# Kernel tuning notes

Hardware: AMD Instinct MI355X
Metric: run time of the kernel (lower is better)

The kernel has to match this reference:

```python
import jax, jax.numpy as jnp
import numpy as np
import math

DM, DP, P = 1024, 128, 256
B, S = 8, 4096

def setup_inputs() -> dict:
    key = jax.random.key(0)
    ks = jax.random.split(key, 7)
    sd = lambda fan_in: 1.0 / math.sqrt(fan_in)
    return {
        "x": jax.random.normal(ks[0], (B, S, DM), jnp.float32),
        "prim_embeds": jax.random.normal(ks[1], (P, DP), jnp.float32),
        "Wq": jax.random.normal(ks[2], (DP, DM), jnp.float32) * sd(DM),
        "Wk": jax.random.normal(ks[3], (DP, DP), jnp.float32) * sd(DP),
        "Wv": jax.random.normal(ks[4], (DP, DP), jnp.float32) * sd(DP),
        "Wo": jax.random.normal(ks[5], (DM, DP), jnp.float32) * sd(DP),
        "gate_w": jax.random.normal(ks[6], (1, DM), jnp.float32) * sd(DM),
        "gate_b": jnp.zeros((1,), jnp.float32),
    }

def reference(x, prim_embeds, Wq, Wk, Wv, Wo, gate_w, gate_b):
    # q: [B,S,dp]; k,v: [P,dp]
    q = jnp.einsum('bsm,pm->bsp', x, Wq)          # p here = d_prim
    k = prim_embeds @ Wk.T                         # [P, dp]
    v = prim_embeds @ Wv.T                         # [P, dp]
    scale = 1.0 / math.sqrt(q.shape[-1])
    scores = jnp.einsum('bsd,pd->bsp', q, k) * scale  # [B,S,P]
    attn = jax.nn.softmax(scores, axis=-1)
    ctx = jnp.einsum('bsp,pd->bsd', attn, v)       # [B,S,dp]
    out = jnp.einsum('bsd,md->bsm', ctx, Wo)       # [B,S,dm]
    gate = jax.nn.sigmoid(jnp.einsum('bsm,om->bso', x, gate_w) + gate_b)  # [B,S,1]
    return gate * out
```

## Files before the change

kernel.cpp:

```cpp
#include <hip/hip_runtime.h>
#include <hip/hip_bf16.h>

typedef unsigned short ushort_t;
typedef __attribute__((ext_vector_type(8))) short short8;
typedef __attribute__((ext_vector_type(8))) unsigned short ushort8;
typedef __attribute__((ext_vector_type(4))) float f32x4;

#define MFMA16(a,b,c) __builtin_amdgcn_mfma_f32_16x16x32_bf16((a),(b),(c),0,0,0)

__device__ __forceinline__ ushort_t f2bf(float f) {
  unsigned int u = __builtin_bit_cast(unsigned int, f);
  u += 0x7FFFu + ((u >> 16) & 1u);
  return (ushort_t)(u >> 16);
}
__device__ __forceinline__ unsigned int pack2bf(float a, float b) {
  unsigned int ua = __builtin_bit_cast(unsigned int, a);
  unsigned int ub = __builtin_bit_cast(unsigned int, b);
  ua += 0x7FFFu + ((ua >> 16) & 1u);
  ub += 0x7FFFu + ((ub >> 16) & 1u);
  return (ua >> 16) | (ub & 0xFFFF0000u);
}

#define DMd 1024
#define DPd 128
#define PPd 256

#define KWQ_OFF 0
#define KWQ_SIZE (8*17*4*512)
#define VWO_OFF KWQ_SIZE
#define VWO_SIZE (64*8*512)
#define KV_BYTE_OFF ((size_t)(KWQ_SIZE + VWO_SIZE) * 2)

__global__ __launch_bounds__(256) void prep1_kernel(
    const float* __restrict__ prim, const float* __restrict__ Wk,
    const float* __restrict__ Wv, ushort_t* __restrict__ ws) {
  __shared__ __align__(16) float Wl[128 * 132];
  __shared__ __align__(16) float pl[2 * 128];
  const int t = threadIdx.x;
  const int mat = blockIdx.x & 1;
  const int p0 = (blockIdx.x >> 1) * 2;
  const float* W = mat ? Wv : Wk;
  #pragma unroll
  for (int i = 0; i < 16; ++i) {
    int w = (i * 256 + t) * 4;
    int row = w >> 7, col = w & 127;
    *(float4*)&Wl[row * 132 + col] = *(const float4*)(W + w);
  }
  if (t < 64) {
    int row = t >> 5, col = (t & 31) * 4;
    *(float4*)&pl[row * 128 + col] = *(const float4*)(prim + (p0 + row) * 128 + col);
  }
  __syncthreads();
  const int d = t & 127, slot = t >> 7;
  float a0 = 0.f, a1 = 0.f, a2 = 0.f, a3 = 0.f;
  #pragma unroll
  for (int j = 0; j < 128; j += 4) {
    float4 w4 = *(const float4*)&Wl[d * 132 + j];
    float4 p4 = *(const float4*)&pl[slot * 128 + j];
    a0 += w4.x * p4.x; a1 += w4.y * p4.y; a2 += w4.z * p4.z; a3 += w4.w * p4.w;
  }
  float r = (a0 + a1) + (a2 + a3);
  float* kf = (float*)((char*)ws + KV_BYTE_OFF);
  float* vT = kf + 32768;
  if (mat == 0) kf[(p0 + slot) * 128 + d] = r;
  else          vT[d * 256 + p0 + slot] = r;
}

__global__ __launch_bounds__(256) void prep2_kernel(
    const float* __restrict__ Wq, const float* __restrict__ Wo,
    const float* __restrict__ gate_w, ushort_t* __restrict__ ws) {
  const float* kf = (const float*)((const char*)ws + KV_BYTE_OFF);
  const float* vT = kf + 32768;
  __shared__ __align__(16) float tile[8 * 128];
  const int b = blockIdx.x, t = threadIdx.x;
  float acc[8];
  #pragma unroll
  for (int j = 0; j < 8; ++j) acc[j] = 0.f;
  if (b < 136) {
    const int pt = b >> 2, ms = b & 3;
    const int p0 = pt * 8;
    const int p  = p0 + (t >> 5);
    const int m0 = ms * 256 + (t & 31) * 8;
    if (p0 < 256) {
      *(float4*)&tile[t * 4] = *(const float4*)(kf + p0 * 128 + t * 4);
      __syncthreads();
      const float* kp = &tile[(t >> 5) * 128];
      for (int d = 0; d < 128; d += 4) {
        float4 kv = *(const float4*)&kp[d];
        float4 qa0 = *(const float4*)(Wq + (d + 0) * 1024 + m0);
        float4 qb0 = *(const float4*)(Wq + (d + 0) * 1024 + m0 + 4);
        float4 qa1 = *(const float4*)(Wq + (d + 1) * 1024 + m0);
        float4 qb1 = *(const float4*)(Wq + (d + 1) * 1024 + m0 + 4);
        float4 qa2 = *(const float4*)(Wq + (d + 2) * 1024 + m0);
        float4 qb2 = *(const float4*)(Wq + (d + 2) * 1024 + m0 + 4);
        float4 qa3 = *(const float4*)(Wq + (d + 3) * 1024 + m0);
        float4 qb3 = *(const float4*)(Wq + (d + 3) * 1024 + m0 + 4);
        acc[0] += kv.x*qa0.x + kv.y*qa1.x + kv.z*qa2.x + kv.w*qa3.x;
        acc[1] += kv.x*qa0.y + kv.y*qa1.y + kv.z*qa2.y + kv.w*qa3.y;
        acc[2] += kv.x*qa0.z + kv.y*qa1.z + kv.z*qa2.z + kv.w*qa3.z;
        acc[3] += kv.x*qa0.w + kv.y*qa1.w + kv.z*qa2.w + kv.w*qa3.w;
        acc[4] += kv.x*qb0.x + kv.y*qb1.x + kv.z*qb2.x + kv.w*qb3.x;
        acc[5] += kv.x*qb0.y + kv.y*qb1.y + kv.z*qb2.y + kv.w*qb3.y;
        acc[6] += kv.x*qb0.z + kv.y*qb1.z + kv.z*qb2.z + kv.w*qb3.z;
        acc[7] += kv.x*qb0.w + kv.y*qb1.w + kv.z*qb2.w + kv.w*qb3.w;
      }
    } else if (p == 256) {
      #pragma unroll
      for (int j = 0; j < 8; ++j) acc[j] = gate_w[m0 + j];
    }
    const int c = m0 >> 7, ct = p >> 4, k4 = (m0 >> 5) & 3;
    const int row = ((m0 >> 3) & 3) * 16 + (p & 15);
    ushort8 u;
    #pragma unroll
    for (int j = 0; j < 8; ++j) u[j] = f2bf(acc[j]);
    *(ushort8*)&ws[KWQ_OFF + ((size_t)(c * 17 + ct) * 4 + k4) * 512 + (size_t)row * 8] = u;
  } else {
    const int mb  = b - 136;
    const int m0t = mb * 8;
    const int m   = m0t + (t >> 5);
    const int p8  = (t & 31) * 8;
    *(float4*)&tile[t * 4] = *(const float4*)(Wo + (size_t)m0t * 128 + t * 4);
    __syncthreads();
    const float* wo = &tile[(t >> 5) * 128];
    for (int d = 0; d < 128; d += 4) {
      float4 wv = *(const float4*)&wo[d];
      float4 va0 = *(const float4*)(vT + (d + 0) * 256 + p8);
      float4 vb0 = *(const float4*)(vT + (d + 0) * 256 + p8 + 4);
      float4 va1 = *(const float4*)(vT + (d + 1) * 256 + p8);
      float4 vb1 = *(const float4*)(vT + (d + 1) * 256 + p8 + 4);
      float4 va2 = *(const float4*)(vT + (d + 2) * 256 + p8);
      float4 vb2 = *(const float4*)(vT + (d + 2) * 256 + p8 + 4);
      float4 va3 = *(const float4*)(vT + (d + 3) * 256 + p8);
      float4 vb3 = *(const float4*)(vT + (d + 3) * 256 + p8 + 4);
      acc[0] += wv.x*va0.x + wv.y*va1.x + wv.z*va2.x + wv.w*va3.x;
      acc[1] += wv.x*va0.y + wv.y*va1.y + wv.z*va2.y + wv.w*va3.y;
      acc[2] += wv.x*va0.z + wv.y*va1.z + wv.z*va2.z + wv.w*va3.z;
      acc[3] += wv.x*va0.w + wv.y*va1.w + wv.z*va2.w + wv.w*va3.w;
      acc[4] += wv.x*vb0.x + wv.y*vb1.x + wv.z*vb2.x + wv.w*vb3.x;
      acc[5] += wv.x*vb0.y + wv.y*vb1.y + wv.z*vb2.y + wv.w*vb3.y;
      acc[6] += wv.x*vb0.z + wv.y*vb1.z + wv.z*vb2.z + wv.w*vb3.z;
      acc[7] += wv.x*vb0.w + wv.y*vb1.w + wv.z*vb2.w + wv.w*vb3.w;
    }
    const int ctg = m >> 4, k8 = p8 >> 5;
    const int row = ((p8 >> 3) & 3) * 16 + (m & 15);
    ushort8 u;
    #pragma unroll
    for (int j = 0; j < 8; ++j) u[j] = f2bf(acc[j]);
    *(ushort8*)&ws[VWO_OFF + ((size_t)(ctg * 8 + k8) * 512) + (size_t)row * 8] = u;
  }
}

#define LDX 136
#define LDSLAB 264

__global__ __launch_bounds__(256, 4) void scores_kernel(
    const float* __restrict__ x, const float* __restrict__ gate_b,
    const ushort_t* __restrict__ ws, float* __restrict__ out)
{
  __shared__ __align__(16) char smem[2 * 32 * LDX * 2 + 32 * 4 * 4 * 2 + 32 * 4];
  ushort_t* xt0      = (ushort_t*)smem;
  ushort_t* xt1      = xt0 + 32 * LDX;
  ushort_t* slab     = (ushort_t*)smem;
  float*    pmax     = (float*)(smem + 2 * 32 * LDX * 2);
  float*    psum     = pmax + 128;
  float*    gate_lds = psum + 128;

  const int t = threadIdx.x, wid = t >> 6, lane = t & 63;
  const int quad = lane >> 4, l16 = lane & 15;
  const int tok0 = blockIdx.x * 32;

  f32x4 acc[2][5];
  #pragma unroll
  for (int rt = 0; rt < 2; ++rt)
    #pragma unroll
    for (int ctl = 0; ctl < 5; ++ctl) acc[rt][ctl] = (f32x4){0.f,0.f,0.f,0.f};

  #pragma unroll
  for (int i = 0; i < 4; ++i) {
    int flat = i * 1024 + t * 4;
    int row = flat >> 7, col = flat & 127;
    float4 fv = *(const float4*)(x + (size_t)(tok0 + row) * 1024 + col);
    unsigned int pk0 = pack2bf(fv.x, fv.y), pk1 = pack2bf(fv.z, fv.w);
    *(unsigned long long*)&xt0[row * LDX + col] =
        (unsigned long long)pk0 | ((unsigned long long)pk1 << 32);
  }
  __syncthreads();

  for (int c = 0; c < 8; ++c) {
    ushort_t* cur = (c & 1) ? xt1 : xt0;
    ushort_t* nxt = (c & 1) ? xt0 : xt1;
    float4 fv[4];
    if (c < 7) {
      #pragma unroll
      for (int i = 0; i < 4; ++i) {
        int flat = i * 1024 + t * 4;
        int row = flat >> 7, col = flat & 127;
        fv[i] = *(const float4*)(x + (size_t)(tok0 + row) * 1024 + (c + 1) * 128 + col);
      }
    }
    #pragma unroll
    for (int k4 = 0; k4 < 4; ++k4) {
      short8 a[2];
      #pragma unroll
      for (int rt = 0; rt < 2; ++rt)
        a[rt] = *(const short8*)&cur[(rt * 16 + l16) * LDX + k4 * 32 + quad * 8];
      #pragma unroll
      for (int ctl = 0; ctl < 5; ++ctl) {
        if (ctl == 4 && wid != 3) continue;
        const int ct = wid * 4 + ctl;
        short8 bfr = *(const short8*)&ws[KWQ_OFF +
            ((size_t)(c * 17 + ct) * 4 + k4) * 512 + (size_t)lane * 8];
        #pragma unroll
        for (int rt = 0; rt < 2; ++rt) acc[rt][ctl] = MFMA16(a[rt], bfr, acc[rt][ctl]);
      }
    }
    if (c < 7) {
      #pragma unroll
      for (int i = 0; i < 4; ++i) {
        int flat = i * 1024 + t * 4;
        int row = flat >> 7, col = flat & 127;
        unsigned int pk0 = pack2bf(fv[i].x, fv[i].y), pk1 = pack2bf(fv[i].z, fv[i].w);
        *(unsigned long long*)&nxt[row * LDX + col] =
            (unsigned long long)pk0 | ((unsigned long long)pk1 << 32);
      }
      __syncthreads();
    }
  }

  const float SC = 0.08838834764831845f * 1.44269504088896f;
  #pragma unroll
  for (int rt = 0; rt < 2; ++rt)
    #pragma unroll
    for (int r = 0; r < 4; ++r) {
      float m = acc[rt][0][r];
      #pragma unroll
      for (int ctl = 1; ctl < 4; ++ctl) m = fmaxf(m, acc[rt][ctl][r]);
      #pragma unroll
      for (int msk = 1; msk < 16; msk <<= 1) m = fmaxf(m, __shfl_xor(m, msk, 64));
      if (l16 == 0) pmax[(rt * 16 + quad * 4 + r) * 4 + wid] = m;
    }
  __syncthreads();
  float Mf[2][4];
  #pragma unroll
  for (int rt = 0; rt < 2; ++rt)
    #pragma unroll
    for (int r = 0; r < 4; ++r) {
      f32x4 pm = *(f32x4*)&pmax[(rt * 16 + quad * 4 + r) * 4];
      Mf[rt][r] = fmaxf(fmaxf(pm[0], pm[1]), fmaxf(pm[2], pm[3]));
    }
  float Sm[2][4];
  #pragma unroll
  for (int rt = 0; rt < 2; ++rt)
    #pragma unroll
    for (int r = 0; r < 4; ++r) Sm[rt][r] = 0.f;
  #pragma unroll
  for (int rt = 0; rt < 2; ++rt)
    #pragma unroll
    for (int ctl = 0; ctl < 4; ++ctl)
      #pragma unroll
      for (int r = 0; r < 4; ++r) {
        float e = exp2f((acc[rt][ctl][r] - Mf[rt][r]) * SC);
        acc[rt][ctl][r] = e;
        Sm[rt][r] += e;
      }
  #pragma unroll
  for (int rt = 0; rt < 2; ++rt)
    #pragma unroll
    for (int r = 0; r < 4; ++r) {
      #pragma unroll
      for (int msk = 1; msk < 16; msk <<= 1) Sm[rt][r] += __shfl_xor(Sm[rt][r], msk, 64);
    }
  if (l16 == 0) {
    #pragma unroll
    for (int rt = 0; rt < 2; ++rt)
      #pragma unroll
      for (int r = 0; r < 4; ++r)
        psum[(rt * 16 + quad * 4 + r) * 4 + wid] = Sm[rt][r];
    if (wid == 3) {
      float gb = gate_b[0];
      #pragma unroll
      for (int rt = 0; rt < 2; ++rt)
        #pragma unroll
        for (int r = 0; r < 4; ++r) {
          float lg = acc[rt][4][r] + gb;
          gate_lds[rt * 16 + quad * 4 + r] = 1.f / (1.f + __expf(-lg));
        }
    }
  }
  __syncthreads();
  float scl[2][4];
  #pragma unroll
  for (int rt = 0; rt < 2; ++rt)
    #pragma unroll
    for (int r = 0; r < 4; ++r) {
      f32x4 ps = *(f32x4*)&psum[(rt * 16 + quad * 4 + r) * 4];
      float g = gate_lds[rt * 16 + quad * 4 + r];
      scl[rt][r] = g / (ps[0] + ps[1] + ps[2] + ps[3]);
    }

  #pragma unroll
  for (int rt = 0; rt < 2; ++rt)
    #pragma unroll
    for (int ctl = 0; ctl < 4; ++ctl)
      #pragma unroll
      for (int r = 0; r < 4; ++r)
        slab[(rt * 16 + quad * 4 + r) * LDSLAB + (wid * 4 + ctl) * 16 + l16] =
            f2bf(acc[rt][ctl][r] * scl[rt][r]);
  __syncthreads();

  #pragma unroll
  for (int j = 0; j < 4; ++j) {
    int flat = j * 1024 + t * 4;
    int row = flat >> 7, col = flat & 127;
    uint4 v = *(const uint4*)&slab[row * LDSLAB + col * 2];
    *(uint4*)&out[(size_t)(tok0 + row) * 1024 + 896 + col] = v;
  }
}

__global__ __launch_bounds__(256, 4) void out_kernel(
    const ushort_t* __restrict__ ws, float* __restrict__ out)
{
  __shared__ __align__(16) ushort_t slab[32 * LDSLAB];
  const int t = threadIdx.x, wid = t >> 6, lane = t & 63;
  const int quad = lane >> 4, l16 = lane & 15;
  const int tok0 = blockIdx.x * 32;

  #pragma unroll
  for (int j = 0; j < 4; ++j) {
    int flat = j * 1024 + t * 4;
    int row = flat >> 7, col = flat & 127;
    uint4 v = *(const uint4*)&out[(size_t)(tok0 + row) * 1024 + 896 + col];
    *(uint4*)&slab[row * LDSLAB + col * 2] = v;
  }
  __syncthreads();

  short8 af[2][8];
  #pragma unroll
  for (int rt = 0; rt < 2; ++rt)
    #pragma unroll
    for (int k8 = 0; k8 < 8; ++k8)
      af[rt][k8] = *(const short8*)&slab[(rt * 16 + l16) * LDSLAB + k8 * 32 + quad * 8];

  const int n0 = wid * 256;
  for (int nt = 0; nt < 16; ++nt) {
    const int ctg = (n0 >> 4) + nt;
    short8 bf[8];
    #pragma unroll
    for (int k8 = 0; k8 < 8; ++k8)
      bf[k8] = *(const short8*)&ws[VWO_OFF + ((size_t)(ctg * 8 + k8) * 512) + (size_t)lane * 8];
    f32x4 oa[2];
    #pragma unroll
    for (int rt = 0; rt < 2; ++rt) oa[rt] = (f32x4){0.f,0.f,0.f,0.f};
    #pragma unroll
    for (int rt = 0; rt < 2; ++rt)
      #pragma unroll
      for (int k8 = 0; k8 < 8; ++k8)
        oa[rt] = MFMA16(af[rt][k8], bf[k8], oa[rt]);
    #pragma unroll
    for (int rt = 0; rt < 2; ++rt)
      #pragma unroll
      for (int r = 0; r < 4; ++r)
        __builtin_nontemporal_store(oa[rt][r],
            &out[(size_t)(tok0 + rt * 16 + quad * 4 + r) * 1024 + n0 + nt * 16 + l16]);
  }
}

extern "C" void kernel_launch(void* const* d_in, const int* in_sizes, int n_in,
                              void* d_out, int out_size, void* d_ws, size_t ws_size,
                              hipStream_t stream) {
  const float* x    = (const float*)d_in[0];
  const float* prim = (const float*)d_in[1];
  const float* Wq   = (const float*)d_in[2];
  const float* Wk   = (const float*)d_in[3];
  const float* Wv   = (const float*)d_in[4];
  const float* Wo   = (const float*)d_in[5];
  const float* gw   = (const float*)d_in[6];
  const float* gb   = (const float*)d_in[7];
  float* out = (float*)d_out;
  ushort_t* ws = (ushort_t*)d_ws;

  prep1_kernel<<<256, 256, 0, stream>>>(prim, Wk, Wv, ws);
  prep2_kernel<<<264, 256, 0, stream>>>(Wq, Wo, gw, ws);
  scores_kernel<<<1024, 256, 0, stream>>>(x, gb, ws, out);
  out_kernel<<<1024, 256, 0, stream>>>(ws, out);
}
```

Before: 327.8 us.

## Stage x tiles with async global-to-LDS loads and convert to bf16 at fragment read

Replaces the register round-trip for x (global load to registers, bf16 pack, LDS store) with asynchronous global_load_lds copies. These put raw fp32 rows into LDS under an XOR swizzle to avoid bank conflicts. The bf16 packing now happens when each wave reads its MFMA A fragments. The conditional fifth column tile is removed, so every wave issues five MFMA column tiles. The intent is to cut VGPR pressure and instruction overhead on the load path and overlap the next chunk's fetch with compute. The costs are double the LDS footprint, redundant MFMA work for three waves, and reliance on the barrier waiting for the async LDS writes to finish.

```diff
diff --git a/kernel.cpp b/kernel.cpp
--- a/kernel.cpp
+++ b/kernel.cpp
@@ -5,6 +5,7 @@
 typedef __attribute__((ext_vector_type(8))) short short8;
 typedef __attribute__((ext_vector_type(8))) unsigned short ushort8;
 typedef __attribute__((ext_vector_type(4))) float f32x4;
+typedef __attribute__((ext_vector_type(4))) unsigned int u32x4;
 
 #define MFMA16(a,b,c) __builtin_amdgcn_mfma_f32_16x16x32_bf16((a),(b),(c),0,0,0)
 
@@ -19,6 +20,17 @@
   ua += 0x7FFFu + ((ua >> 16) & 1u);
   ub += 0x7FFFu + ((ub >> 16) & 1u);
   return (ua >> 16) | (ub & 0xFFFF0000u);
+}
+__device__ __forceinline__ short8 pack8(float4 lo, float4 hi) {
+  u32x4 u;
+  u.x = pack2bf(lo.x, lo.y); u.y = pack2bf(lo.z, lo.w);
+  u.z = pack2bf(hi.x, hi.y); u.w = pack2bf(hi.z, hi.w);
+  return __builtin_bit_cast(short8, u);
+}
+__device__ __forceinline__ void gl_lds16(const float* g, void* lds) {
+  __builtin_amdgcn_global_load_lds(
+      (__attribute__((address_space(1))) void*)(g),
+      (__attribute__((address_space(3))) void*)(lds), 16, 0, 0);
 }
 
 #define DMd 1024
@@ -150,24 +162,24 @@
   }
 }
 
-#define LDX 136
 #define LDSLAB 264
 
 __global__ __launch_bounds__(256, 4) void scores_kernel(
     const float* __restrict__ x, const float* __restrict__ gate_b,
     const ushort_t* __restrict__ ws, float* __restrict__ out)
 {
-  __shared__ __align__(16) char smem[2 * 32 * LDX * 2 + 32 * 4 * 4 * 2 + 32 * 4];
-  ushort_t* xt0      = (ushort_t*)smem;
-  ushort_t* xt1      = xt0 + 32 * LDX;
+  __shared__ __align__(16) char smem[32768 + 32 * 4 * 4 * 2 + 32 * 4];
+  char*     xb0      = smem;
+  char*     xb1      = smem + 16384;
   ushort_t* slab     = (ushort_t*)smem;
-  float*    pmax     = (float*)(smem + 2 * 32 * LDX * 2);
+  float*    pmax     = (float*)(smem + 32768);
   float*    psum     = pmax + 128;
   float*    gate_lds = psum + 128;
 
   const int t = threadIdx.x, wid = t >> 6, lane = t & 63;
   const int quad = lane >> 4, l16 = lane & 15;
   const int tok0 = blockIdx.x * 32;
+  const int ct0 = wid * 4;
 
   f32x4 acc[2][5];
   #pragma unroll
@@ -175,56 +187,63 @@
     #pragma unroll
     for (int ctl = 0; ctl < 5; ++ctl) acc[rt][ctl] = (f32x4){0.f,0.f,0.f,0.f};
 
+  int srow[4], scol[4], sobase[4];
   #pragma unroll
   for (int i = 0; i < 4; ++i) {
-    int flat = i * 1024 + t * 4;
-    int row = flat >> 7, col = flat & 127;
-    float4 fv = *(const float4*)(x + (size_t)(tok0 + row) * 1024 + col);
-    unsigned int pk0 = pack2bf(fv.x, fv.y), pk1 = pack2bf(fv.z, fv.w);
-    *(unsigned long long*)&xt0[row * LDX + col] =
-        (unsigned long long)pk0 | ((unsigned long long)pk1 << 32);
-  }
+    int obase = (wid * 4 + i) * 1024;
+    int o = obase + lane * 16;
+    int row = o >> 9;
+    int cb  = o & 511;
+    int scb = cb ^ ((row & 7) << 4);
+    srow[i] = row; scol[i] = scb >> 2; sobase[i] = obase;
+  }
+
+  #define STAGE(buf, cc)                                                       \
+    {                                                                          \
+      _Pragma("unroll")                                                        \
+      for (int i = 0; i < 4; ++i)                                              \
+        gl_lds16(x + (size_t)(tok0 + srow[i]) * 1024 + (cc) * 128 + scol[i],   \
+                 (buf) + sobase[i]);                                           \
+    }
+
+  const int f    = (l16 & 7) << 4;
+  const int rb0  = l16 * 512;
+  const int rb1  = (16 + l16) * 512;
+
+  STAGE(xb0, 0)
   __syncthreads();
 
   for (int c = 0; c < 8; ++c) {
-    ushort_t* cur = (c & 1) ? xt1 : xt0;
-    ushort_t* nxt = (c & 1) ? xt0 : xt1;
-    float4 fv[4];
-    if (c < 7) {
-      #pragma unroll
-      for (int i = 0; i < 4; ++i) {
-        int flat = i * 1024 + t * 4;
-        int row = flat >> 7, col = flat & 127;
-        fv[i] = *(const float4*)(x + (size_t)(tok0 + row) * 1024 + (c + 1) * 128 + col);
-      }
-    }
+    const char* xb = (c & 1) ? xb1 : xb0;
+    char*      nxt = (c & 1) ? xb0 : xb1;
+    if (c < 7) STAGE(nxt, c + 1)
+    const ushort_t* wb = ws + KWQ_OFF + (size_t)(c * 17) * 4 * 512 + (size_t)lane * 8;
     #pragma unroll
     for (int k4 = 0; k4 < 4; ++k4) {
-      short8 a[2];
-      #pragma unroll
-      for (int rt = 0; rt < 2; ++rt)
-        a[rt] = *(const short8*)&cur[(rt * 16 + l16) * LDX + k4 * 32 + quad * 8];
-      #pragma unroll
-      for (int ctl = 0; ctl < 5; ++ctl) {
-        if (ctl == 4 && wid != 3) continue;
-        const int ct = wid * 4 + ctl;
-        short8 bfr = *(const short8*)&ws[KWQ_OFF +
-            ((size_t)(c * 17 + ct) * 4 + k4) * 512 + (size_t)lane * 8];
-        #pragma unroll
-        for (int rt = 0; rt < 2; ++rt) acc[rt][ctl] = MFMA16(a[rt], bfr, acc[rt][ctl]);
-      }
-    }
-    if (c < 7) {
-      #pragma unroll
-      for (int i = 0; i < 4; ++i) {
-        int flat = i * 1024 + t * 4;
-        int row = flat >> 7, col = flat & 127;
-        unsigned int pk0 = pack2bf(fv[i].x, fv[i].y), pk1 = pack2bf(fv[i].z, fv[i].w);
-        *(unsigned long long*)&nxt[row * LDX + col] =
-            (unsigned long long)pk0 | ((unsigned long long)pk1 << 32);
-      }
-      __syncthreads();
-    }
+      const int cb0 = k4 * 128 + quad * 32;
+      float4 a0lo = *(const float4*)(xb + rb0 + ((cb0     ) ^ f));
+      float4 a0hi = *(const float4*)(xb + rb0 + ((cb0 + 16) ^ f));
+      float4 a1lo = *(const float4*)(xb + rb1 + ((cb0     ) ^ f));
+      float4 a1hi = *(const float4*)(xb + rb1 + ((cb0 + 16) ^ f));
+      short8 b0 = *(const short8*)&wb[(size_t)((ct0 + 0) * 4 + k4) * 512];
+      short8 b1 = *(const short8*)&wb[(size_t)((ct0 + 1) * 4 + k4) * 512];
+      short8 b2 = *(const short8*)&wb[(size_t)((ct0 + 2) * 4 + k4) * 512];
+      short8 b3 = *(const short8*)&wb[(size_t)((ct0 + 3) * 4 + k4) * 512];
+      short8 b4 = *(const short8*)&wb[(size_t)((ct0 + 4) * 4 + k4) * 512];
+      short8 a0 = pack8(a0lo, a0hi);
+      short8 a1 = pack8(a1lo, a1hi);
+      acc[0][0] = MFMA16(a0, b0, acc[0][0]);
+      acc[1][0] = MFMA16(a1, b0, acc[1][0]);
+      acc[0][1] = MFMA16(a0, b1, acc[0][1]);
+      acc[1][1] = MFMA16(a1, b1, acc[1][1]);
+      acc[0][2] = MFMA16(a0, b2, acc[0][2]);
+      acc[1][2] = MFMA16(a1, b2, acc[1][2]);
+      acc[0][3] = MFMA16(a0, b3, acc[0][3]);
+      acc[1][3] = MFMA16(a1, b3, acc[1][3]);
+      acc[0][4] = MFMA16(a0, b4, acc[0][4]);
+      acc[1][4] = MFMA16(a1, b4, acc[1][4]);
+    }
+    __syncthreads();
   }
 
   const float SC = 0.08838834764831845f * 1.44269504088896f;
@@ -304,7 +323,7 @@
     for (int ctl = 0; ctl < 4; ++ctl)
       #pragma unroll
       for (int r = 0; r < 4; ++r)
-        slab[(rt * 16 + quad * 4 + r) * LDSLAB + (wid * 4 + ctl) * 16 + l16] =
+        slab[(rt * 16 + quad * 4 + r) * LDSLAB + (ct0 + ctl) * 16 + l16] =
             f2bf(acc[rt][ctl][r] * scl[rt][r]);
   __syncthreads();
 
```

New measurement: 318.6 us. -2.8%, faster.
